# Optimization experiments

Hardware: AMD Instinct MI355X
Metric: run time of the kernel (lower is better)

## Reference

```python
import jax, jax.numpy as jnp
import numpy as np

B, H, W, C = 8, 64, 64, 384
HEADS, WS = 12, 14
KD = C // HEADS          # key_dim = 32
D = KD                    # attn_ratio = 1 -> d = key_dim
DH = D * HEADS            # = 384
HID = 4 * C               # mlp hidden = 1536
SCALE = KD ** -0.5
EPS = 1e-5
N = WS * WS               # 196 tokens per window


def _bias_idx():
    pts = [(i, j) for i in range(WS) for j in range(WS)]
    off, idxs = {}, []
    for p1 in pts:
        for p2 in pts:
            o = (abs(p1[0] - p2[0]), abs(p1[1] - p2[1]))
            if o not in off:
                off[o] = len(off)
            idxs.append(off[o])
    return np.asarray(idxs, np.int32).reshape(N, N), len(off)


def setup_inputs() -> dict:
    key = jax.random.key(0)
    ks = jax.random.split(key, 8)
    bias_idx_np, n_off = _bias_idx()  # n_off == 196 for a 14x14 window
    s = 0.02
    return {
        "x": jax.random.normal(ks[0], (B, H * W, C), jnp.float32),
        "ln_attn_w": jnp.ones((C,), jnp.float32),
        "ln_attn_b": jnp.zeros((C,), jnp.float32),
        "qkv_w": jax.random.normal(ks[1], (3 * DH, C), jnp.float32) * s,
        "qkv_b": jnp.zeros((3 * DH,), jnp.float32),
        "proj_w": jax.random.normal(ks[2], (C, DH), jnp.float32) * s,
        "proj_b": jnp.zeros((C,), jnp.float32),
        "attn_biases": jax.random.normal(ks[3], (HEADS, n_off), jnp.float32) * s,
        "conv_w": jax.random.normal(ks[4], (C, 1, 3, 3), jnp.float32) * s,  # depthwise OIHW
        "bn_w": jnp.ones((C,), jnp.float32),
        "bn_b": jnp.zeros((C,), jnp.float32),
        "bn_mean": jnp.zeros((C,), jnp.float32),
        "bn_var": jnp.ones((C,), jnp.float32),
        "ln_mlp_w": jnp.ones((C,), jnp.float32),
        "ln_mlp_b": jnp.zeros((C,), jnp.float32),
        "fc1_w": jax.random.normal(ks[5], (HID, C), jnp.float32) * s,
        "fc1_b": jnp.zeros((HID,), jnp.float32),
        "fc2_w": jax.random.normal(ks[6], (C, HID), jnp.float32) * s,
        "fc2_b": jnp.zeros((C,), jnp.float32),
        "bias_idx": jnp.asarray(bias_idx_np),
    }


def _ln(x, w, b):
    m = jnp.mean(x, -1, keepdims=True)
    v = jnp.mean((x - m) ** 2, -1, keepdims=True)
    return (x - m) * jax.lax.rsqrt(v + EPS) * w + b


def reference(x, ln_attn_w, ln_attn_b, qkv_w, qkv_b, proj_w, proj_b, attn_biases,
              conv_w, bn_w, bn_b, bn_mean, bn_var, ln_mlp_w, ln_mlp_b,
              fc1_w, fc1_b, fc2_w, fc2_b, bias_idx):
    L = H * W
    res = x
    # ---- window partition (pad 64 -> 70, 5x5 windows of 14x14) ----
    pad = (-H) % WS
    pH = H + pad
    n = pH // WS
    xw = x.reshape(B, H, W, C)
    xw = jnp.pad(xw, ((0, 0), (0, pad), (0, pad), (0, 0)))
    xw = xw.reshape(B, n, WS, n, WS, C).transpose(0, 1, 3, 2, 4, 5)
    xw = xw.reshape(B * n * n, N, C)
    # ---- attention with relative-position bias ----
    xn = _ln(xw, ln_attn_w, ln_attn_b)
    qkv = xn @ qkv_w.T + qkv_b                       # [Bw, N, 3*DH]
    qkv = qkv.reshape(-1, N, HEADS, 3 * KD)
    q, k, v = qkv[..., :KD], qkv[..., KD:2 * KD], qkv[..., 2 * KD:]
    bias = attn_biases[:, bias_idx]                  # [HEADS, N, N]
    attn = jnp.einsum('bnhd,bmhd->bhnm', q, k) * SCALE + bias[None]
    attn = jax.nn.softmax(attn, axis=-1)
    out = jnp.einsum('bhnm,bmhd->bnhd', attn, v).reshape(-1, N, DH)
    out = out @ proj_w.T + proj_b
    # ---- window reverse + crop + residual ----
    out = out.reshape(B, n, n, WS, WS, C).transpose(0, 1, 3, 2, 4, 5)
    out = out.reshape(B, pH, pH, C)[:, :H, :W]
    x = res + out.reshape(B, L, C)
    # ---- depthwise local conv + BN (eval mode) ----
    xc = x.reshape(B, H, W, C).transpose(0, 3, 1, 2)  # NCHW
    xc = jax.lax.conv_general_dilated(xc, conv_w, (1, 1), 'SAME',
                                      feature_group_count=C)
    inv = jax.lax.rsqrt(bn_var + 1e-5)
    xc = (xc - bn_mean[None, :, None, None]) * (inv * bn_w)[None, :, None, None] \
         + bn_b[None, :, None, None]
    x = xc.reshape(B, C, L).transpose(0, 2, 1)
    # ---- MLP (LN -> fc1 -> GELU(exact) -> fc2) + residual ----
    h = _ln(x, ln_mlp_w, ln_mlp_b)
    h = jax.nn.gelu(h @ fc1_w.T + fc1_b, approximate=False)
    h = h @ fc2_w.T + fc2_b
    return x + h
```

## Files before the change

kernel.cpp:

```cpp
#include <hip/hip_runtime.h>
#include <hip/hip_bf16.h>

#define DI __device__ __forceinline__

typedef __attribute__((ext_vector_type(8))) __bf16 bf16x8;
typedef __attribute__((ext_vector_type(4))) float f32x4;
typedef __attribute__((ext_vector_type(2))) float f32x2;
typedef __attribute__((ext_vector_type(8))) unsigned short us8;
typedef __attribute__((ext_vector_type(4))) unsigned short us4;

constexpr int CBATCH = 8;
constexpr int HW = 64;
constexpr int CDIM = 384;
constexpr int HEADS = 12;
constexpr int WS = 14;
constexpr int NTOK = 196;
constexpr int NWIN = 200;
constexpr int MV = 39200;
constexpr int MPAD = 39296;
constexpr int NQKV = 1152;
constexpr int HIDD = 1536;
constexpr int MMLP = 32768;
constexpr int NBIAS = 12 * 13 * 13 * 4 * 16 * 4;
constexpr int PLSTR = 228;
constexpr float SCALE = 0.17677669529663687f;

DI unsigned short f2bf(float f) { __bf16 b = (__bf16)f; return __builtin_bit_cast(unsigned short, b); }
DI bf16x8 ldfrag(const unsigned short* p) { return __builtin_bit_cast(bf16x8, *(const us8*)p); }
DI f32x4 mfma16(bf16x8 a, bf16x8 b, f32x4 c) {
  return __builtin_amdgcn_mfma_f32_16x16x32_bf16(a, b, c, 0, 0, 0);
}
DI void async16(const void* g, void* l) {
  __builtin_amdgcn_global_load_lds((const __attribute__((address_space(1))) void*)g,
                                   (__attribute__((address_space(3))) void*)l, 16, 0, 0);
}
DI int vt_addr(int d, int t) {
  return d * 256 + (((t & ~7) ^ ((d & 7) << 3) ^ (((d >> 3) & 3) << 5)) | (t & 7));
}

__global__ __launch_bounds__(256) void k_cvt(const float* __restrict__ s,
                                             unsigned short* __restrict__ d, int n) {
  int i = blockIdx.x * 256 + threadIdx.x;
  if (i < n) d[i] = f2bf(s[i]);
}

__global__ __launch_bounds__(256) void k_bias2(const float* __restrict__ ab,
                                               const int* __restrict__ bidx,
                                               float* __restrict__ bt, int n_off) {
  int i = blockIdx.x * 256 + threadIdx.x;
  if (i >= NBIAS) return;
  int r = i & 3, l15 = (i >> 2) & 15, g = (i >> 6) & 3;
  int j = i >> 8;
  int kt = j % 13;
  int j2 = j / 13;
  int qt = j2 % 13;
  int h = j2 / 13;
  int q = qt * 16 + l15, k = kt * 16 + g * 4 + r;
  float v = 0.f;
  if (q < 196 && k < 196) v = ab[h * n_off + bidx[q * 196 + k]];
  bt[i] = v;
}

template <int WIN>
__global__ __launch_bounds__(256) void k_ln(const float* __restrict__ src,
                                            const float* __restrict__ lw,
                                            const float* __restrict__ lb,
                                            unsigned short* __restrict__ dst) {
  const int row = blockIdx.x * 4 + (threadIdx.x >> 6);
  const int l = threadIdx.x & 63;
  const int c0 = l * 6;
  const float* p;
  bool valid;
  if (WIN) {
    int win = row / 196, t = row - win * 196;
    int b = win / 25, wi = win - b * 25;
    int wr = wi / 5, wc = wi - wr * 5;
    int hh = wr * 14 + t / 14, ww = wc * 14 + (t - (t / 14) * 14);
    valid = (row < MV) && (hh < HW) && (ww < HW);
    p = src + ((size_t)b * 4096 + hh * 64 + ww) * CDIM;
  } else {
    valid = true;
    p = src + (size_t)row * CDIM;
  }
  float v[6];
  if (valid) {
    f32x2 a = *(const f32x2*)(p + c0);
    f32x2 b2 = *(const f32x2*)(p + c0 + 2);
    f32x2 c2 = *(const f32x2*)(p + c0 + 4);
    v[0] = a.x; v[1] = a.y; v[2] = b2.x; v[3] = b2.y; v[4] = c2.x; v[5] = c2.y;
  } else {
#pragma unroll
    for (int k = 0; k < 6; ++k) v[k] = 0.f;
  }
  float s = 0.f, q = 0.f;
#pragma unroll
  for (int k = 0; k < 6; ++k) { s += v[k]; q += v[k] * v[k]; }
#pragma unroll
  for (int m = 1; m <= 32; m <<= 1) {
    s += __shfl_xor(s, m, 64);
    q += __shfl_xor(q, m, 64);
  }
  float mean = s * (1.0f / 384.0f);
  float var = q * (1.0f / 384.0f) - mean * mean;
  float rs = rsqrtf(var + 1e-5f);
#pragma unroll
  for (int k = 0; k < 6; ++k) {
    float y = (v[k] - mean) * rs * lw[c0 + k] + lb[c0 + k];
    dst[(size_t)row * CDIM + c0 + k] = f2bf(y);
  }
}

__global__ __launch_bounds__(256) void k_conv(const float* __restrict__ x1,
                                              const float* __restrict__ cw,
                                              const float* __restrict__ bw,
                                              const float* __restrict__ bb,
                                              const float* __restrict__ bm,
                                              const float* __restrict__ bv,
                                              float* __restrict__ x2) {
  int idx = blockIdx.x * 256 + threadIdx.x;
  int c = idx % 384;
  int x = (idx / 384) & 63;
  int b = idx / (384 * 64);
  const float* base = x1 + (size_t)b * 4096 * 384 + c;
  float w[9];
#pragma unroll
  for (int k = 0; k < 9; ++k) w[k] = cw[c * 9 + k];
  float sc = rsqrtf(bv[c] + 1e-5f) * bw[c];
  float sb = bb[c] - bm[c] * sc;
  float t0m = 0.f, t0c = 0.f, t0p = 0.f;
  float t1m, t1c, t1p, t2m, t2c, t2p;
  t1m = (x > 0) ? base[(x - 1) * 384] : 0.f;
  t1c = base[x * 384];
  t1p = (x < 63) ? base[(x + 1) * 384] : 0.f;
  for (int y = 0; y < 64; ++y) {
    if (y < 63) {
      int ro = (y + 1) * 64;
      t2m = (x > 0) ? base[(ro + x - 1) * 384] : 0.f;
      t2c = base[(ro + x) * 384];
      t2p = (x < 63) ? base[(ro + x + 1) * 384] : 0.f;
    } else { t2m = t2c = t2p = 0.f; }
    float o = w[0] * t0m + w[1] * t0c + w[2] * t0p +
              w[3] * t1m + w[4] * t1c + w[5] * t1p +
              w[6] * t2m + w[7] * t2c + w[8] * t2p;
    x2[((size_t)b * 4096 + y * 64 + x) * 384 + c] = o * sc + sb;
    t0m = t1m; t0c = t1c; t0p = t1p;
    t1m = t2m; t1c = t2c; t1p = t2p;
  }
}

__global__ __launch_bounds__(256, 4) void k_attn(const unsigned short* __restrict__ qkv,
                                                 const float* __restrict__ bias_f,
                                                 unsigned short* __restrict__ aout) {
  __shared__ unsigned short Vt[32 * 256];
  __shared__ unsigned short Pl[4][16 * PLSTR];
  const int bid = blockIdx.x;
  const int blk = (bid & 7) * 300 + (bid >> 3);
  const int win = blk / 12, h = blk - win * 12;
  const int tid = threadIdx.x;
  const int w = tid >> 6, l = tid & 63;
  const int l15 = l & 15, g = l >> 4;
  const unsigned short* qb = qkv + (size_t)win * 196 * 1152 + h * 96;

  for (int i = tid; i < 896; i += 256) {
    int t = i >> 2, d8 = (i & 3) << 3;
    us8 z = {0, 0, 0, 0, 0, 0, 0, 0};
    if (t < 196) z = *(const us8*)(qb + (size_t)t * 1152 + 64 + d8);
#pragma unroll
    for (int j = 0; j < 8; ++j) Vt[vt_addr(d8 + j, t)] = z[j];
  }
  for (int z = l; z < 16 * 20; z += 64) {
    int rr = z / 20, cc = 208 + (z - rr * 20);
    Pl[w][rr * PLSTR + cc] = 0;
  }
  __syncthreads();

  const float* bth = bias_f + (size_t)h * (13 * 13 * 4 * 16 * 4);
  unsigned short* plw = &Pl[w][0];
  for (int qt = w; qt < 13; qt += 4) {
    bf16x8 aq = ldfrag(qb + (size_t)(qt * 16 + l15) * 1152 + g * 8);
    float su = 0.f;
#pragma unroll
    for (int kt = 0; kt < 13; ++kt) {
      f32x4 zz = {0.f, 0.f, 0.f, 0.f};
      bf16x8 bk = ldfrag(qb + (size_t)(kt * 16 + l15) * 1152 + 32 + g * 8);
      f32x4 s = mfma16(bk, aq, zz);
      f32x4 bb = *(const f32x4*)(bth + (size_t)(((qt * 13 + kt) * 4 + g) * 16 + l15) * 4);
      us4 pk;
#pragma unroll
      for (int r = 0; r < 4; ++r) {
        float p = __expf(s[r] + bb[r]);
        if (kt == 12 && g != 0) p = 0.f;
        su += p;
        pk[r] = f2bf(p);
      }
      *(us4*)(plw + l15 * PLSTR + kt * 16 + g * 4) = pk;
    }
    su += __shfl_xor(su, 16, 64);
    su += __shfl_xor(su, 32, 64);
    asm volatile("s_waitcnt lgkmcnt(0)" ::: "memory");
    __builtin_amdgcn_sched_barrier(0);
    f32x4 o0 = {0.f, 0.f, 0.f, 0.f}, o1 = {0.f, 0.f, 0.f, 0.f};
#pragma unroll
    for (int kc = 0; kc < 7; ++kc) {
      int t0 = kc * 32 + g * 8;
      bf16x8 pa = ldfrag(plw + l15 * PLSTR + t0);
      bf16x8 b0 = ldfrag(&Vt[vt_addr(l15, t0)]);
      bf16x8 b1 = ldfrag(&Vt[vt_addr(16 + l15, t0)]);
      o0 = mfma16(pa, b0, o0);
      o1 = mfma16(pa, b1, o1);
    }
    float inv = 1.0f / su;
#pragma unroll
    for (int r = 0; r < 4; ++r) {
      int rw = qt * 16 + g * 4 + r;
      if (rw < 196) {
        size_t rb = ((size_t)win * 196 + rw) * 384 + h * 32;
        aout[rb + l15] = f2bf(o0[r] * inv);
        aout[rb + 16 + l15] = f2bf(o1[r] * inv);
      }
    }
  }
}

template <int MODE>
__global__ __launch_bounds__(256) void k_gemm(const unsigned short* __restrict__ A,
                                              const unsigned short* __restrict__ B,
                                              const float* __restrict__ bias,
                                              const float* __restrict__ auxr,
                                              float* __restrict__ auxw,
                                              unsigned short* __restrict__ outb,
                                              int K) {
  __shared__ unsigned short As[128 * 64];
  __shared__ unsigned short Bs[128 * 64];
  const int tid = threadIdx.x;
  const int w = tid >> 6, l = tid & 63;
  const int l15 = l & 15, g = l >> 4;
  const int wm = w >> 1, wn = w & 1;
  const size_t arow0 = (size_t)blockIdx.x * 128;
  const size_t brow0 = (size_t)blockIdx.y * 128;
  f32x4 acc[4][4] = {};
  for (int ks = 0; ks < K; ks += 64) {
    if (ks) __syncthreads();
#pragma unroll
    for (int it = 0; it < 4; ++it) {
      const int f = it * 256 + tid;
      const int r = f >> 3, c8 = (f & 7) << 3;
      const int lb = (it * 256 + w * 64) * 8;
      async16(A + (arow0 + r) * K + ks + c8, &As[lb]);
      async16(B + (brow0 + r) * K + ks + c8, &Bs[lb]);
    }
    __syncthreads();
#pragma unroll
    for (int kk = 0; kk < 2; ++kk) {
      bf16x8 af[4], bfr[4];
#pragma unroll
      for (int i = 0; i < 4; ++i)
        af[i] = ldfrag(&As[(wm * 64 + i * 16 + l15) * 64 + kk * 32 + g * 8]);
#pragma unroll
      for (int j = 0; j < 4; ++j)
        bfr[j] = ldfrag(&Bs[(wn * 64 + j * 16 + l15) * 64 + kk * 32 + g * 8]);
#pragma unroll
      for (int i = 0; i < 4; ++i)
#pragma unroll
        for (int j = 0; j < 4; ++j)
          acc[i][j] = mfma16(af[i], bfr[j], acc[i][j]);
    }
  }
#pragma unroll
  for (int i = 0; i < 4; ++i) {
#pragma unroll
    for (int j = 0; j < 4; ++j) {
#pragma unroll
      for (int r = 0; r < 4; ++r) {
        const int row = (int)arow0 + wm * 64 + i * 16 + g * 4 + r;
        const int col = (int)brow0 + wn * 64 + j * 16 + l15;
        float v = acc[i][j][r] + bias[col];
        if (MODE == 0) {
          int ch = col % 96;
          float o = (ch < 32) ? v * SCALE : v;
          outb[(size_t)row * NQKV + col] = f2bf(o);
        } else if (MODE == 1) {
          if (row < MV) {
            int win = row / 196, t = row - win * 196;
            int b = win / 25, wi = win - b * 25;
            int wr = wi / 5, wc = wi - wr * 5;
            int hh = wr * 14 + t / 14, ww = wc * 14 + (t - (t / 14) * 14);
            if (hh < HW && ww < HW) {
              size_t di = ((size_t)b * 4096 + hh * 64 + ww) * 384 + col;
              auxw[di] = auxr[di] + v;
            }
          }
        } else if (MODE == 2) {
          float gl = 0.5f * v * (1.0f + erff(v * 0.7071067811865475f));
          outb[(size_t)row * HIDD + col] = f2bf(gl);
        } else {
          size_t di = (size_t)row * 384 + col;
          auxw[di] = auxr[di] + v;
        }
      }
    }
  }
}

extern "C" void kernel_launch(void* const* d_in, const int* in_sizes, int n_in,
                              void* d_out, int out_size, void* d_ws, size_t ws_size,
                              hipStream_t stream) {
  const float* x = (const float*)d_in[0];
  const float* ln_attn_w = (const float*)d_in[1];
  const float* ln_attn_b = (const float*)d_in[2];
  const float* qkv_w = (const float*)d_in[3];
  const float* qkv_b = (const float*)d_in[4];
  const float* proj_w = (const float*)d_in[5];
  const float* proj_b = (const float*)d_in[6];
  const float* attn_biases = (const float*)d_in[7];
  const float* conv_w = (const float*)d_in[8];
  const float* bn_w = (const float*)d_in[9];
  const float* bn_b = (const float*)d_in[10];
  const float* bn_mean = (const float*)d_in[11];
  const float* bn_var = (const float*)d_in[12];
  const float* ln_mlp_w = (const float*)d_in[13];
  const float* ln_mlp_b = (const float*)d_in[14];
  const float* fc1_w = (const float*)d_in[15];
  const float* fc1_b = (const float*)d_in[16];
  const float* fc2_w = (const float*)d_in[17];
  const float* fc2_b = (const float*)d_in[18];
  const int* bias_idx = (const int*)d_in[19];

  char* ws = (char*)d_ws;
  size_t off = 0;
  auto alloc = [&](size_t n) {
    void* p = ws + off;
    off = (off + n + 255) & ~(size_t)255;
    return p;
  };
  unsigned short* xn = (unsigned short*)alloc((size_t)MPAD * CDIM * 2);
  unsigned short* qkv = (unsigned short*)alloc((size_t)MMLP * HIDD * 2);
  unsigned short* attn = (unsigned short*)alloc((size_t)MMLP * CDIM * 4);
  float* x1 = (float*)alloc((size_t)MMLP * CDIM * 4);
  unsigned short* wq = (unsigned short*)alloc((size_t)NQKV * CDIM * 2);
  unsigned short* wp = (unsigned short*)alloc((size_t)CDIM * CDIM * 2);
  unsigned short* w1 = (unsigned short*)alloc((size_t)HIDD * CDIM * 2);
  unsigned short* w2 = (unsigned short*)alloc((size_t)CDIM * HIDD * 2);
  float* bias_f = (float*)alloc((size_t)NBIAS * 4);
  unsigned short* hbuf = qkv;
  float* x2 = (float*)attn;
  unsigned short* xln = xn;
  int n_off = in_sizes[7] / HEADS;

  dim3 B256(256);
  k_cvt<<<dim3((NQKV * CDIM + 255) / 256), B256, 0, stream>>>(qkv_w, wq, NQKV * CDIM);
  k_cvt<<<dim3((CDIM * CDIM + 255) / 256), B256, 0, stream>>>(proj_w, wp, CDIM * CDIM);
  k_cvt<<<dim3((HIDD * CDIM + 255) / 256), B256, 0, stream>>>(fc1_w, w1, HIDD * CDIM);
  k_cvt<<<dim3((CDIM * HIDD + 255) / 256), B256, 0, stream>>>(fc2_w, w2, CDIM * HIDD);
  k_bias2<<<dim3((NBIAS + 255) / 256), B256, 0, stream>>>(attn_biases, bias_idx, bias_f, n_off);
  k_ln<1><<<dim3(MPAD / 4), B256, 0, stream>>>(x, ln_attn_w, ln_attn_b, xn);
  k_gemm<0><<<dim3(MPAD / 128, NQKV / 128), B256, 0, stream>>>(xn, wq, qkv_b, nullptr, nullptr, qkv, CDIM);
  k_attn<<<dim3(NWIN * HEADS), B256, 0, stream>>>(qkv, bias_f, attn);
  k_gemm<1><<<dim3(MPAD / 128, CDIM / 128), B256, 0, stream>>>(attn, wp, proj_b, x, x1, nullptr, CDIM);
  k_conv<<<dim3(CBATCH * HW * CDIM / 256), B256, 0, stream>>>(x1, conv_w, bn_w, bn_b, bn_mean, bn_var, x2);
  k_ln<0><<<dim3(MMLP / 4), B256, 0, stream>>>(x2, ln_mlp_w, ln_mlp_b, xln);
  k_gemm<2><<<dim3(MMLP / 128, HIDD / 128), B256, 0, stream>>>(xln, w1, fc1_b, nullptr, nullptr, hbuf, CDIM);
  k_gemm<3><<<dim3(MMLP / 128, CDIM / 128), B256, 0, stream>>>(hbuf, w2, fc2_b, x2, (float*)d_out, nullptr, HIDD);
}
```

Measured before the change: 617.2 us.

## Use bf16 attention bias, hoist K fragments, remap GEMM blocks per XCD, template K

The relative-position bias table is now stored as bf16 instead of fp32, which halves the bias reads in the attention kernel. K fragments for a window/head are loaded once into registers, and each query tile prefetches all 13 bias vectors up front; occupancy drops from 4 to 3 waves per SIMD to make room for the extra registers. The GEMM remaps block IDs so that consecutive tiles land on the same XCD for better L2 reuse, and it takes K as a template parameter so loops can be fully unrolled. Rounding the bias to bf16 adds a small accuracy risk.

```diff
diff --git a/kernel.cpp b/kernel.cpp
--- a/kernel.cpp
+++ b/kernel.cpp
@@ -26,6 +26,7 @@
 constexpr float SCALE = 0.17677669529663687f;
 
 DI unsigned short f2bf(float f) { __bf16 b = (__bf16)f; return __builtin_bit_cast(unsigned short, b); }
+DI float bf2f(unsigned short u) { unsigned x = (unsigned)u << 16; return __builtin_bit_cast(float, x); }
 DI bf16x8 ldfrag(const unsigned short* p) { return __builtin_bit_cast(bf16x8, *(const us8*)p); }
 DI f32x4 mfma16(bf16x8 a, bf16x8 b, f32x4 c) {
   return __builtin_amdgcn_mfma_f32_16x16x32_bf16(a, b, c, 0, 0, 0);
@@ -46,7 +47,7 @@
 
 __global__ __launch_bounds__(256) void k_bias2(const float* __restrict__ ab,
                                                const int* __restrict__ bidx,
-                                               float* __restrict__ bt, int n_off) {
+                                               unsigned short* __restrict__ bt, int n_off) {
   int i = blockIdx.x * 256 + threadIdx.x;
   if (i >= NBIAS) return;
   int r = i & 3, l15 = (i >> 2) & 15, g = (i >> 6) & 3;
@@ -58,7 +59,7 @@
   int q = qt * 16 + l15, k = kt * 16 + g * 4 + r;
   float v = 0.f;
   if (q < 196 && k < 196) v = ab[h * n_off + bidx[q * 196 + k]];
-  bt[i] = v;
+  bt[i] = f2bf(v);
 }
 
 template <int WIN>
@@ -148,8 +149,8 @@
   }
 }
 
-__global__ __launch_bounds__(256, 4) void k_attn(const unsigned short* __restrict__ qkv,
-                                                 const float* __restrict__ bias_f,
+__global__ __launch_bounds__(256, 3) void k_attn(const unsigned short* __restrict__ qkv,
+                                                 const unsigned short* __restrict__ bias_t,
                                                  unsigned short* __restrict__ aout) {
   __shared__ unsigned short Vt[32 * 256];
   __shared__ unsigned short Pl[4][16 * PLSTR];
@@ -174,21 +175,29 @@
   }
   __syncthreads();
 
-  const float* bth = bias_f + (size_t)h * (13 * 13 * 4 * 16 * 4);
+  bf16x8 bkv[13];
+#pragma unroll
+  for (int kt = 0; kt < 13; ++kt)
+    bkv[kt] = ldfrag(qb + (size_t)(kt * 16 + l15) * 1152 + 32 + g * 8);
+
+  const unsigned short* bth = bias_t + (size_t)h * (13 * 13 * 4 * 16 * 4);
   unsigned short* plw = &Pl[w][0];
   for (int qt = w; qt < 13; qt += 4) {
     bf16x8 aq = ldfrag(qb + (size_t)(qt * 16 + l15) * 1152 + g * 8);
+    us4 bv[13];
+#pragma unroll
+    for (int kt = 0; kt < 13; ++kt)
+      bv[kt] = *(const us4*)(bth + (size_t)(((qt * 13 + kt) * 4 + g) * 16 + l15) * 4);
+
     float su = 0.f;
 #pragma unroll
     for (int kt = 0; kt < 13; ++kt) {
       f32x4 zz = {0.f, 0.f, 0.f, 0.f};
-      bf16x8 bk = ldfrag(qb + (size_t)(kt * 16 + l15) * 1152 + 32 + g * 8);
-      f32x4 s = mfma16(bk, aq, zz);
-      f32x4 bb = *(const f32x4*)(bth + (size_t)(((qt * 13 + kt) * 4 + g) * 16 + l15) * 4);
+      f32x4 s = mfma16(bkv[kt], aq, zz);
       us4 pk;
 #pragma unroll
       for (int r = 0; r < 4; ++r) {
-        float p = __expf(s[r] + bb[r]);
+        float p = __expf(s[r] + bf2f(bv[kt][r]));
         if (kt == 12 && g != 0) p = 0.f;
         su += p;
         pk[r] = f2bf(p);
@@ -222,22 +231,27 @@
   }
 }
 
-template <int MODE>
+template <int MODE, int K>
 __global__ __launch_bounds__(256) void k_gemm(const unsigned short* __restrict__ A,
                                               const unsigned short* __restrict__ B,
                                               const float* __restrict__ bias,
                                               const float* __restrict__ auxr,
                                               float* __restrict__ auxw,
-                                              unsigned short* __restrict__ outb,
-                                              int K) {
+                                              unsigned short* __restrict__ outb) {
   __shared__ unsigned short As[128 * 64];
   __shared__ unsigned short Bs[128 * 64];
   const int tid = threadIdx.x;
   const int w = tid >> 6, l = tid & 63;
   const int l15 = l & 15, g = l >> 4;
   const int wm = w >> 1, wn = w & 1;
-  const size_t arow0 = (size_t)blockIdx.x * 128;
-  const size_t brow0 = (size_t)blockIdx.y * 128;
+  const int nwg = gridDim.x * gridDim.y;
+  const int orig = blockIdx.y * gridDim.x + blockIdx.x;
+  const int cq = nwg >> 3, cr = nwg & 7;
+  const int xcd = orig & 7, cidx = orig >> 3;
+  const int flat = (xcd < cr ? xcd * (cq + 1) : cr * (cq + 1) + (xcd - cr) * cq) + cidx;
+  const int bx = flat % gridDim.x, by = flat / gridDim.x;
+  const size_t arow0 = (size_t)bx * 128;
+  const size_t brow0 = (size_t)by * 128;
   f32x4 acc[4][4] = {};
   for (int ks = 0; ks < K; ks += 64) {
     if (ks) __syncthreads();
@@ -341,7 +355,7 @@
   unsigned short* wp = (unsigned short*)alloc((size_t)CDIM * CDIM * 2);
   unsigned short* w1 = (unsigned short*)alloc((size_t)HIDD * CDIM * 2);
   unsigned short* w2 = (unsigned short*)alloc((size_t)CDIM * HIDD * 2);
-  float* bias_f = (float*)alloc((size_t)NBIAS * 4);
+  unsigned short* bias_t = (unsigned short*)alloc((size_t)NBIAS * 2);
   unsigned short* hbuf = qkv;
   float* x2 = (float*)attn;
   unsigned short* xln = xn;
@@ -352,13 +366,13 @@
   k_cvt<<<dim3((CDIM * CDIM + 255) / 256), B256, 0, stream>>>(proj_w, wp, CDIM * CDIM);
   k_cvt<<<dim3((HIDD * CDIM + 255) / 256), B256, 0, stream>>>(fc1_w, w1, HIDD * CDIM);
   k_cvt<<<dim3((CDIM * HIDD + 255) / 256), B256, 0, stream>>>(fc2_w, w2, CDIM * HIDD);
-  k_bias2<<<dim3((NBIAS + 255) / 256), B256, 0, stream>>>(attn_biases, bias_idx, bias_f, n_off);
+  k_bias2<<<dim3((NBIAS + 255) / 256), B256, 0, stream>>>(attn_biases, bias_idx, bias_t, n_off);
   k_ln<1><<<dim3(MPAD / 4), B256, 0, stream>>>(x, ln_attn_w, ln_attn_b, xn);
-  k_gemm<0><<<dim3(MPAD / 128, NQKV / 128), B256, 0, stream>>>(xn, wq, qkv_b, nullptr, nullptr, qkv, CDIM);
-  k_attn<<<dim3(NWIN * HEADS), B256, 0, stream>>>(qkv, bias_f, attn);
-  k_gemm<1><<<dim3(MPAD / 128, CDIM / 128), B256, 0, stream>>>(attn, wp, proj_b, x, x1, nullptr, CDIM);
+  k_gemm<0, CDIM><<<dim3(MPAD / 128, NQKV / 128), B256, 0, stream>>>(xn, wq, qkv_b, nullptr, nullptr, qkv);
+  k_attn<<<dim3(NWIN * HEADS), B256, 0, stream>>>(qkv, bias_t, attn);
+  k_gemm<1, CDIM><<<dim3(MPAD / 128, CDIM / 128), B256, 0, stream>>>(attn, wp, proj_b, x, x1, nullptr);
   k_conv<<<dim3(CBATCH * HW * CDIM / 256), B256, 0, stream>>>(x1, conv_w, bn_w, bn_b, bn_mean, bn_var, x2);
   k_ln<0><<<dim3(MMLP / 4), B256, 0, stream>>>(x2, ln_mlp_w, ln_mlp_b, xln);
-  k_gemm<2><<<dim3(MMLP / 128, HIDD / 128), B256, 0, stream>>>(xln, w1, fc1_b, nullptr, nullptr, hbuf, CDIM);
-  k_gemm<3><<<dim3(MMLP / 128, CDIM / 128), B256, 0, stream>>>(hbuf, w2, fc2_b, x2, (float*)d_out, nullptr, HIDD);
-}
+  k_gemm<2, CDIM><<<dim3(MMLP / 128, HIDD / 128), B256, 0, stream>>>(xln, w1, fc1_b, nullptr, nullptr, hbuf);
+  k_gemm<3, HIDD><<<dim3(MMLP / 128, CDIM / 128), B256, 0, stream>>>(hbuf, w2, fc2_b, x2, (float*)d_out, nullptr);
+}
```

Measured after the change: 560.2 us. 9.2% less time.
